# Kernel optimization log

Hardware: AMD Instinct MI355X
Metric: run time of the kernel (lower is better)

Reference implementation:

```python
import jax, jax.numpy as jnp
import numpy as np

B, H, S, D = 4, 16, 2048, 64

def setup_inputs() -> dict:
    key = jax.random.key(0)
    kq, kk, kv = jax.random.split(key, 3)
    q = jax.random.normal(kq, (B, H, S, D), dtype=jnp.float32)
    k = jax.random.normal(kk, (B, H, S, D), dtype=jnp.float32)
    v = jax.random.normal(kv, (B, H, S, D), dtype=jnp.float32)
    return {"q": q, "k": k, "v": v}

def reference(q, k, v):
    # dots: [b,h,i,j] = q . k (NO 1/sqrt(d) scaling, matching source)
    dots = jnp.einsum('bhid,bhjd->bhij', q, k)
    # causal=False (and the source's causal mask is a no-op bug anyway)
    attn = jax.nn.softmax(dots, axis=-1)
    # out: [b,h,i,d] = sum_j attn[b,h,i,j] * v[b,h,j,d]
    return jnp.einsum('bhjd,bhij->bhid', v, attn)
```

## Files before the change

kernel.cpp:

```cpp
#include <hip/hip_runtime.h>
#include <hip/hip_bf16.h>
#include <stdint.h>

#define B_ 4
#define H_ 16
#define S_ 2048
#define D_ 64
#define QBLK 128
#define KBLK 64
#define LDW 72
#define LOG2E 1.44269504088896340736f

typedef __attribute__((ext_vector_type(8))) short short8;
typedef __attribute__((ext_vector_type(4))) float f32x4;
typedef __attribute__((ext_vector_type(16))) float f32x16;
typedef _Float16 f16x8 __attribute__((ext_vector_type(8)));
typedef _Float16 f16x4 __attribute__((ext_vector_type(4)));
typedef __fp16 fp16x2 __attribute__((ext_vector_type(2)));

__device__ __forceinline__ unsigned short f2bf(float f) {
  union { float f; unsigned int u; } x; x.f = f;
  unsigned int u = x.u;
  unsigned int r = (u + 0x7FFFu + ((u >> 16) & 1u)) >> 16;
  return (unsigned short)r;
}
__device__ __forceinline__ float bf2f(unsigned short h) {
  union { unsigned int u; float f; } y; y.u = ((unsigned int)h) << 16;
  return y.f;
}

__device__ __forceinline__ unsigned pkrtz(float a, float b) {
  union { fp16x2 h; unsigned u; } c;
  c.h = __builtin_amdgcn_cvt_pkrtz(a, b);
  return c.u;
}
__device__ __forceinline__ fp16x2 u2h(unsigned u) {
  union { unsigned u; fp16x2 h; } c; c.u = u; return c.h;
}

__device__ __forceinline__ float fast_exp2(float x) {
#if __has_builtin(__builtin_amdgcn_exp2f)
  return __builtin_amdgcn_exp2f(x);
#else
  return exp2f(x);
#endif
}

__device__ __forceinline__ void swap32(unsigned &a, unsigned &b) {
#if __has_builtin(__builtin_amdgcn_permlane32_swap)
  typedef int i32x2 __attribute__((ext_vector_type(2)));
  i32x2 r = __builtin_amdgcn_permlane32_swap((int)a, (int)b, false, false);
  a = (unsigned)r[0]; b = (unsigned)r[1];
#else
  unsigned pa = (unsigned)__shfl_xor((int)a, 32);
  unsigned pb = (unsigned)__shfl_xor((int)b, 32);
  bool lo = (threadIdx.x & 32) == 0;
  unsigned r0 = lo ? a : pb;
  unsigned r1 = lo ? pa : b;
  a = r0; b = r1;
#endif
}

__device__ __forceinline__ float pairmax(float x) {
  unsigned a = __float_as_uint(x), b = a;
  swap32(a, b);
  return fmaxf(__uint_as_float(a), __uint_as_float(b));
}
__device__ __forceinline__ float pairsum(float x) {
  unsigned a = __float_as_uint(x), b = a;
  swap32(a, b);
  return __uint_as_float(a) + __uint_as_float(b);
}

#define GLOAD16(g, l) __builtin_amdgcn_global_load_lds( \
    (const __attribute__((address_space(1))) unsigned int*)(g), \
    (__attribute__((address_space(3))) unsigned int*)(l), 16, 0, 0)

__global__ void prep_k(const float* __restrict__ K, _Float16* __restrict__ Kp) {
  int e4 = (blockIdx.x * 256 + threadIdx.x) * 4;
  int bh  = e4 >> 17;
  int rem = e4 & 131071;
  int s   = rem >> 6;
  int d0  = rem & 63;
  const float4 kv = *(const float4*)(K + (size_t)e4);
  f16x4 h;
  h[0] = (_Float16)kv.x; h[1] = (_Float16)kv.y;
  h[2] = (_Float16)kv.z; h[3] = (_Float16)kv.w;
  size_t off = ((size_t)bh * S_ + s) * 128 + (unsigned)((d0 * 2) ^ ((s & 7) << 4));
  *(f16x4*)((char*)Kp + off) = h;
}

__global__ void prep_v(const float* __restrict__ V, _Float16* __restrict__ Vt) {
  __shared__ _Float16 tile[64][66];
  int bh = blockIdx.x >> 5;
  int st = blockIdx.x & 31;
  const float* Vb = V + ((size_t)bh * S_ + st * 64) * 64;
  int tid = threadIdx.x;
  #pragma unroll
  for (int i = 0; i < 4; ++i) {
    int idx = i * 1024 + tid * 4;
    int r = idx >> 6, c = idx & 63;
    float4 vv = *(const float4*)(Vb + (size_t)r * 64 + c);
    f16x4 o;
    o[0] = (_Float16)vv.x; o[1] = (_Float16)vv.y;
    o[2] = (_Float16)vv.z; o[3] = (_Float16)vv.w;
    *(f16x4*)&tile[r][c] = o;
  }
  __syncthreads();
  int chunk = tid & 15;
  int dbase = tid >> 4;
  size_t outb = (size_t)bh * (64 * S_ * 2) + (size_t)st * 128;
  #pragma unroll
  for (int i = 0; i < 4; ++i) {
    int d = dbase + i * 16;
    f16x4 o;
    o[0] = tile[chunk * 4 + 0][d];
    o[1] = tile[chunk * 4 + 1][d];
    o[2] = tile[chunk * 4 + 2][d];
    o[3] = tile[chunk * 4 + 3][d];
    size_t off = outb + (size_t)d * (S_ * 2) + (unsigned)((chunk * 8) ^ ((d & 7) << 4));
    *(f16x4*)((char*)Vt + off) = o;
  }
}

__global__ __launch_bounds__(256)
void attn_fwd4(const float* __restrict__ Q, const _Float16* __restrict__ Kg,
               const _Float16* __restrict__ Vg, float* __restrict__ O) {
  __shared__ char smem[32768];

  const int tid  = threadIdx.x;
  const int lane = tid & 63;
  const int wid  = tid >> 6;
  const int l31  = lane & 31;
  const int hi   = lane >> 5;

  const int qtile = blockIdx.x;
  const int bh    = blockIdx.y;

  const char* KB = (const char*)Kg + (size_t)bh * (S_ * 128);
  const char* VB = (const char*)Vg + (size_t)bh * (64 * S_ * 2);
  const float* Qb = Q + (size_t)bh * S_ * D_;
  float*       Ob = O + (size_t)bh * S_ * D_;

  const int qrow = qtile * QBLK + wid * 32 + l31;
  f16x8 qf[4];
  #pragma unroll
  for (int ds = 0; ds < 4; ++ds) {
    const float* qp = Qb + (size_t)qrow * D_ + ds * 16 + hi * 8;
    float4 a = *(const float4*)(qp);
    float4 b = *(const float4*)(qp + 4);
    qf[ds][0] = (_Float16)(a.x * LOG2E); qf[ds][1] = (_Float16)(a.y * LOG2E);
    qf[ds][2] = (_Float16)(a.z * LOG2E); qf[ds][3] = (_Float16)(a.w * LOG2E);
    qf[ds][4] = (_Float16)(b.x * LOG2E); qf[ds][5] = (_Float16)(b.y * LOG2E);
    qf[ds][6] = (_Float16)(b.z * LOG2E); qf[ds][7] = (_Float16)(b.w * LOG2E);
  }

  f32x16 oacc[2];
  #pragma unroll
  for (int dn = 0; dn < 2; ++dn)
    #pragma unroll
    for (int r = 0; r < 16; ++r) oacc[dn][r] = 0.f;
  float m_r = -INFINITY, l_r = 0.f;

  f32x16 zero16;
  #pragma unroll
  for (int r = 0; r < 16; ++r) zero16[r] = 0.f;

  #define STAGE(buf, kb)                                                        \
    {                                                                           \
      char* Kl_ = smem + (buf) * 16384;                                         \
      char* Vl_ = Kl_ + 8192;                                                   \
      _Pragma("unroll")                                                         \
      for (int c = 0; c < 4; ++c) {                                             \
        int id = c * 4 + wid;                                                   \
        if (id < 8) {                                                           \
          GLOAD16(KB + (size_t)(kb) * 128 + id * 1024 + lane * 16,              \
                  Kl_ + id * 1024);                                             \
        } else {                                                                \
          int i = id - 8;                                                       \
          GLOAD16(VB + (size_t)(i * 8 + (lane >> 3)) * (S_ * 2)                 \
                     + ((kb) >> 6) * 128 + (lane & 7) * 16,                     \
                  Vl_ + i * 1024);                                              \
        }                                                                       \
      }                                                                         \
    }

  STAGE(0, 0);
  __syncthreads();

  for (int it = 0; it < S_ / KBLK; ++it) {
    const int cur = it & 1;
    if (it < S_ / KBLK - 1) STAGE(cur ^ 1, (it + 1) * KBLK);

    const char* Kl = smem + cur * 16384;
    const char* Vl = Kl + 8192;

    f32x16 sacc_a, sacc_b;
    __builtin_amdgcn_s_setprio(1);
    {
      const int row = l31;
      const int sw = (row & 7) << 4;
      sacc_a = __builtin_amdgcn_mfma_f32_32x32x16_f16(
          *(const f16x8*)(Kl + row * 128 + ((0) ^ sw)), qf[0], zero16, 0, 0, 0);
      sacc_a = __builtin_amdgcn_mfma_f32_32x32x16_f16(
          *(const f16x8*)(Kl + row * 128 + ((32 + hi * 16) ^ sw) - hi * 16 + hi * 16), qf[1], sacc_a, 0, 0, 0);
      sacc_a = __builtin_amdgcn_mfma_f32_32x32x16_f16(
          *(const f16x8*)(Kl + row * 128 + ((64 + hi * 16) ^ sw) - hi * 16 + hi * 16), qf[2], sacc_a, 0, 0, 0);
      sacc_a = __builtin_amdgcn_mfma_f32_32x32x16_f16(
          *(const f16x8*)(Kl + row * 128 + ((96 + hi * 16) ^ sw) - hi * 16 + hi * 16), qf[3], sacc_a, 0, 0, 0);
    }
    __builtin_amdgcn_s_setprio(0);
    {
      const int row = l31;
      const int sw = (row & 7) << 4;
      sacc_a = __builtin_amdgcn_mfma_f32_32x32x16_f16(
          *(const f16x8*)(Kl + row * 128 + ((0 * 32 + hi * 16) ^ sw)), qf[0], zero16, 0, 0, 0);
      #pragma unroll
      for (int ds = 1; ds < 4; ++ds)
        sacc_a = __builtin_amdgcn_mfma_f32_32x32x16_f16(
            *(const f16x8*)(Kl + row * 128 + ((ds * 32 + hi * 16) ^ sw)), qf[ds], sacc_a, 0, 0, 0);
    }
    {
      const int row = 32 + l31;
      const int sw = (row & 7) << 4;
      sacc_b = __builtin_amdgcn_mfma_f32_32x32x16_f16(
          *(const f16x8*)(Kl + row * 128 + ((0 * 32 + hi * 16) ^ sw)), qf[0], zero16, 0, 0, 0);
      #pragma unroll
      for (int ds = 1; ds < 4; ++ds)
        sacc_b = __builtin_amdgcn_mfma_f32_32x32x16_f16(
            *(const f16x8*)(Kl + row * 128 + ((ds * 32 + hi * 16) ^ sw)), qf[ds], sacc_b, 0, 0, 0);
    }

    {
      float v0 = fmaxf(fmaxf(sacc_a[0], sacc_a[1]), sacc_a[2]);
      float v1 = fmaxf(fmaxf(sacc_a[3], sacc_a[4]), sacc_a[5]);
      float v2 = fmaxf(fmaxf(sacc_a[6], sacc_a[7]), sacc_a[8]);
      float v3 = fmaxf(fmaxf(sacc_a[9], sacc_a[10]), sacc_a[11]);
      float v4 = fmaxf(fmaxf(sacc_a[12], sacc_a[13]), sacc_a[14]);
      float w0 = fmaxf(fmaxf(v0, v1), v2);
      float w1 = fmaxf(fmaxf(v3, v4), sacc_a[15]);
      float mx = pairmax(fmaxf(w0, w1));
      if (!__all(mx <= m_r + 8.f)) {
        float nm = fmaxf(m_r, mx);
        float sc = fast_exp2(m_r - nm);
        m_r = nm; l_r *= sc;
        #pragma unroll
        for (int dn = 0; dn < 2; ++dn)
          #pragma unroll
          for (int r = 0; r < 16; ++r) oacc[dn][r] *= sc;
      }
      unsigned ww[8];
      #pragma unroll
      for (int r1 = 0; r1 < 4; ++r1) {
        float p0 = fast_exp2(sacc_a[4 * r1 + 0] - m_r);
        float p1 = fast_exp2(sacc_a[4 * r1 + 1] - m_r);
        float p2 = fast_exp2(sacc_a[4 * r1 + 2] - m_r);
        float p3 = fast_exp2(sacc_a[4 * r1 + 3] - m_r);
        ww[r1 * 2 + 0] = pkrtz(p0, p1);
        ww[r1 * 2 + 1] = pkrtz(p2, p3);
      }
      {
        const fp16x2 ones = {(__fp16)1.f, (__fp16)1.f};
        float rA = __builtin_amdgcn_fdot2(u2h(ww[0]), ones, 0.f, false);
        float rB = __builtin_amdgcn_fdot2(u2h(ww[1]), ones, 0.f, false);
        rA = __builtin_amdgcn_fdot2(u2h(ww[2]), ones, rA, false);
        rB = __builtin_amdgcn_fdot2(u2h(ww[3]), ones, rB, false);
        rA = __builtin_amdgcn_fdot2(u2h(ww[4]), ones, rA, false);
        rB = __builtin_amdgcn_fdot2(u2h(ww[5]), ones, rB, false);
        rA = __builtin_amdgcn_fdot2(u2h(ww[6]), ones, rA, false);
        rB = __builtin_amdgcn_fdot2(u2h(ww[7]), ones, rB, false);
        l_r += rA + rB;
      }
      f16x8 pb0, pb1;
      {
        unsigned u0 = ww[0], u1 = ww[1], u2 = ww[2], u3 = ww[3];
        swap32(u0, u2); swap32(u1, u3);
        union { unsigned u[4]; f16x8 v; } c;
        c.u[0] = u0; c.u[1] = u1; c.u[2] = u2; c.u[3] = u3;
        pb0 = c.v;
      }
      {
        unsigned u0 = ww[4], u1 = ww[5], u2 = ww[6], u3 = ww[7];
        swap32(u0, u2); swap32(u1, u3);
        union { unsigned u[4]; f16x8 v; } c;
        c.u[0] = u0; c.u[1] = u1; c.u[2] = u2; c.u[3] = u3;
        pb1 = c.v;
      }
      __builtin_amdgcn_s_setprio(1);
      #pragma unroll
      for (int dn = 0; dn < 2; ++dn) {
        const int d = dn * 32 + l31;
        const int sw = (d & 7) << 4;
        f16x8 vf0 = *(const f16x8*)(Vl + d * 128 + ((0 * 32 + hi * 16) ^ sw));
        f16x8 vf1 = *(const f16x8*)(Vl + d * 128 + ((1 * 32 + hi * 16) ^ sw));
        oacc[dn] = __builtin_amdgcn_mfma_f32_32x32x16_f16(vf0, pb0, oacc[dn], 0, 0, 0);
        oacc[dn] = __builtin_amdgcn_mfma_f32_32x32x16_f16(vf1, pb1, oacc[dn], 0, 0, 0);
      }
      __builtin_amdgcn_s_setprio(0);
    }

    {
      float v0 = fmaxf(fmaxf(sacc_b[0], sacc_b[1]), sacc_b[2]);
      float v1 = fmaxf(fmaxf(sacc_b[3], sacc_b[4]), sacc_b[5]);
      float v2 = fmaxf(fmaxf(sacc_b[6], sacc_b[7]), sacc_b[8]);
      float v3 = fmaxf(fmaxf(sacc_b[9], sacc_b[10]), sacc_b[11]);
      float v4 = fmaxf(fmaxf(sacc_b[12], sacc_b[13]), sacc_b[14]);
      float w0 = fmaxf(fmaxf(v0, v1), v2);
      float w1 = fmaxf(fmaxf(v3, v4), sacc_b[15]);
      float mx = pairmax(fmaxf(w0, w1));
      if (!__all(mx <= m_r + 8.f)) {
        float nm = fmaxf(m_r, mx);
        float sc = fast_exp2(m_r - nm);
        m_r = nm; l_r *= sc;
        #pragma unroll
        for (int dn = 0; dn < 2; ++dn)
          #pragma unroll
          for (int r = 0; r < 16; ++r) oacc[dn][r] *= sc;
      }
      unsigned ww[8];
      #pragma unroll
      for (int r1 = 0; r1 < 4; ++r1) {
        float p0 = fast_exp2(sacc_b[4 * r1 + 0] - m_r);
        float p1 = fast_exp2(sacc_b[4 * r1 + 1] - m_r);
        float p2 = fast_exp2(sacc_b[4 * r1 + 2] - m_r);
        float p3 = fast_exp2(sacc_b[4 * r1 + 3] - m_r);
        ww[r1 * 2 + 0] = pkrtz(p0, p1);
        ww[r1 * 2 + 1] = pkrtz(p2, p3);
      }
      {
        const fp16x2 ones = {(__fp16)1.f, (__fp16)1.f};
        float rA = __builtin_amdgcn_fdot2(u2h(ww[0]), ones, 0.f, false);
        float rB = __builtin_amdgcn_fdot2(u2h(ww[1]), ones, 0.f, false);
        rA = __builtin_amdgcn_fdot2(u2h(ww[2]), ones, rA, false);
        rB = __builtin_amdgcn_fdot2(u2h(ww[3]), ones, rB, false);
        rA = __builtin_amdgcn_fdot2(u2h(ww[4]), ones, rA, false);
        rB = __builtin_amdgcn_fdot2(u2h(ww[5]), ones, rB, false);
        rA = __builtin_amdgcn_fdot2(u2h(ww[6]), ones, rA, false);
        rB = __builtin_amdgcn_fdot2(u2h(ww[7]), ones, rB, false);
        l_r += rA + rB;
      }
      f16x8 pb2, pb3;
      {
        unsigned u0 = ww[0], u1 = ww[1], u2 = ww[2], u3 = ww[3];
        swap32(u0, u2); swap32(u1, u3);
        union { unsigned u[4]; f16x8 v; } c;
        c.u[0] = u0; c.u[1] = u1; c.u[2] = u2; c.u[3] = u3;
        pb2 = c.v;
      }
      {
        unsigned u0 = ww[4], u1 = ww[5], u2 = ww[6], u3 = ww[7];
        swap32(u0, u2); swap32(u1, u3);
        union { unsigned u[4]; f16x8 v; } c;
        c.u[0] = u0; c.u[1] = u1; c.u[2] = u2; c.u[3] = u3;
        pb3 = c.v;
      }
      __builtin_amdgcn_s_setprio(1);
      #pragma unroll
      for (int dn = 0; dn < 2; ++dn) {
        const int d = dn * 32 + l31;
        const int sw = (d & 7) << 4;
        f16x8 vf2 = *(const f16x8*)(Vl + d * 128 + ((2 * 32 + hi * 16) ^ sw));
        f16x8 vf3 = *(const f16x8*)(Vl + d * 128 + ((3 * 32 + hi * 16) ^ sw));
        oacc[dn] = __builtin_amdgcn_mfma_f32_32x32x16_f16(vf2, pb2, oacc[dn], 0, 0, 0);
        oacc[dn] = __builtin_amdgcn_mfma_f32_32x32x16_f16(vf3, pb3, oacc[dn], 0, 0, 0);
      }
      __builtin_amdgcn_s_setprio(0);
    }

    __syncthreads();
  }
  #undef STAGE

  const float inv = 1.0f / pairsum(l_r);
  float* Ep = (float*)(smem + wid * 8192);
  #pragma unroll
  for (int dn = 0; dn < 2; ++dn)
    #pragma unroll
    for (int r = 0; r < 16; ++r) {
      int d = dn * 32 + (r & 3) + 8 * (r >> 2) + 4 * hi;
      Ep[d * 32 + l31] = oacc[dn][r] * inv;
    }
  __syncthreads();
  const int q2 = lane >> 1, dh = lane & 1;
  float* orow = Ob + (size_t)(qtile * QBLK + wid * 32 + q2) * D_ + dh * 32;
  #pragma unroll
  for (int c = 0; c < 8; ++c) {
    float4 o4;
    o4.x = Ep[(dh * 32 + c * 4 + 0) * 32 + q2];
    o4.y = Ep[(dh * 32 + c * 4 + 1) * 32 + q2];
    o4.z = Ep[(dh * 32 + c * 4 + 2) * 32 + q2];
    o4.w = Ep[(dh * 32 + c * 4 + 3) * 32 + q2];
    *(float4*)(orow + c * 4) = o4;
  }
}

__global__ __launch_bounds__(256, 2)
void attn_fwd(const float* __restrict__ Q, const float* __restrict__ K,
              const float* __restrict__ V, float* __restrict__ O) {
  __shared__ alignas(16) unsigned short Kh_lds[KBLK * LDW];
  __shared__ alignas(16) unsigned short Kl_lds[KBLK * LDW];
  __shared__ alignas(16) unsigned short Vt_lds[D_ * LDW];
  __shared__ alignas(16) unsigned short P_lds[4][16 * LDW];

  const int tid  = threadIdx.x;
  const int lane = tid & 63;
  const int wid  = tid >> 6;
  const int l15  = lane & 15;
  const int dgrp = lane >> 4;

  const int qtile = blockIdx.x;
  const int bh    = blockIdx.y;

  const size_t base = (size_t)bh * S_ * D_;
  const float* Qb = Q + base;
  const float* Kb = K + base;
  const float* Vb = V + base;
  float*       Ob = O + base;

  const int qrow = qtile * 64 + wid * 16 + l15;
  short8 qfh[2], qfl[2];
  {
    const float* qp = Qb + (size_t)qrow * D_ + dgrp * 8;
    #pragma unroll
    for (int s = 0; s < 2; ++s)
      #pragma unroll
      for (int j = 0; j < 8; ++j) {
        float f = qp[s * 32 + j];
        unsigned short h = f2bf(f);
        qfh[s][j] = (short)h;
        qfl[s][j] = (short)f2bf(f - bf2f(h));
      }
  }

  f32x4 oacc[4];
  #pragma unroll
  for (int t = 0; t < 4; ++t) oacc[t] = f32x4{0.f, 0.f, 0.f, 0.f};
  float m_r[4], l_r[4];
  #pragma unroll
  for (int j = 0; j < 4; ++j) { m_r[j] = -INFINITY; l_r[j] = 0.f; }

  for (int kb = 0; kb < S_; kb += KBLK) {
    __syncthreads();
    #pragma unroll
    for (int c = 0; c < 4; ++c) {
      int e = (c * 256 + tid) * 4;
      int r = e >> 6, col = e & 63;
      const float4 kv = *(const float4*)(Kb + (size_t)(kb + r) * D_ + col);
      ushort4 kh, kl;
      kh.x = f2bf(kv.x); kl.x = f2bf(kv.x - bf2f(kh.x));
      kh.y = f2bf(kv.y); kl.y = f2bf(kv.y - bf2f(kh.y));
      kh.z = f2bf(kv.z); kl.z = f2bf(kv.z - bf2f(kh.z));
      kh.w = f2bf(kv.w); kl.w = f2bf(kv.w - bf2f(kh.w));
      *(ushort4*)&Kh_lds[r * LDW + col] = kh;
      *(ushort4*)&Kl_lds[r * LDW + col] = kl;
      const float4 vv = *(const float4*)(Vb + (size_t)(kb + r) * D_ + col);
      Vt_lds[(col + 0) * LDW + r] = f2bf(vv.x);
      Vt_lds[(col + 1) * LDW + r] = f2bf(vv.y);
      Vt_lds[(col + 2) * LDW + r] = f2bf(vv.z);
      Vt_lds[(col + 3) * LDW + r] = f2bf(vv.w);
    }
    __syncthreads();

    f32x4 sa[4];
    #pragma unroll
    for (int t = 0; t < 4; ++t) {
      sa[t] = f32x4{0.f, 0.f, 0.f, 0.f};
      #pragma unroll
      for (int s = 0; s < 2; ++s) {
        const int off = (t * 16 + l15) * LDW + s * 32 + dgrp * 8;
        short8 kfh = *(const short8*)&Kh_lds[off];
        short8 kfl = *(const short8*)&Kl_lds[off];
        sa[t] = __builtin_amdgcn_mfma_f32_16x16x32_bf16(qfh[s], kfh, sa[t], 0, 0, 0);
        sa[t] = __builtin_amdgcn_mfma_f32_16x16x32_bf16(qfh[s], kfl, sa[t], 0, 0, 0);
        sa[t] = __builtin_amdgcn_mfma_f32_16x16x32_bf16(qfl[s], kfh, sa[t], 0, 0, 0);
      }
    }

    float pmax[4];
    #pragma unroll
    for (int j = 0; j < 4; ++j) {
      float mx = fmaxf(fmaxf(sa[0][j], sa[1][j]), fmaxf(sa[2][j], sa[3][j]));
      #pragma unroll
      for (int m = 1; m < 16; m <<= 1) mx = fmaxf(mx, __shfl_xor(mx, m));
      pmax[j] = mx;
    }
    float scale[4];
    #pragma unroll
    for (int j = 0; j < 4; ++j) {
      float nm = fmaxf(m_r[j], pmax[j]);
      scale[j] = __expf(m_r[j] - nm);
      m_r[j] = nm;
    }
    float rs[4] = {0.f, 0.f, 0.f, 0.f};
    #pragma unroll
    for (int t = 0; t < 4; ++t)
      #pragma unroll
      for (int j = 0; j < 4; ++j) {
        float p = __expf(sa[t][j] - m_r[j]);
        rs[j] += p;
        P_lds[wid][(dgrp * 4 + j) * LDW + t * 16 + l15] = f2bf(p);
      }
    #pragma unroll
    for (int j = 0; j < 4; ++j) {
      #pragma unroll
      for (int m = 1; m < 16; m <<= 1) rs[j] += __shfl_xor(rs[j], m);
      l_r[j] = l_r[j] * scale[j] + rs[j];
      #pragma unroll
      for (int t = 0; t < 4; ++t) oacc[t][j] *= scale[j];
    }

    #pragma unroll
    for (int s = 0; s < 2; ++s) {
      short8 pf = *(const short8*)&P_lds[wid][l15 * LDW + s * 32 + dgrp * 8];
      #pragma unroll
      for (int t = 0; t < 4; ++t) {
        short8 vf = *(const short8*)&Vt_lds[(t * 16 + l15) * LDW + s * 32 + dgrp * 8];
        oacc[t] = __builtin_amdgcn_mfma_f32_16x16x32_bf16(pf, vf, oacc[t], 0, 0, 0);
      }
    }
  }

  #pragma unroll
  for (int j = 0; j < 4; ++j) {
    float inv = 1.0f / l_r[j];
    int row = qtile * 64 + wid * 16 + dgrp * 4 + j;
    float* op = Ob + (size_t)row * D_ + l15;
    #pragma unroll
    for (int t = 0; t < 4; ++t)
      op[t * 16] = oacc[t][j] * inv;
  }
}

extern "C" void kernel_launch(void* const* d_in, const int* in_sizes, int n_in,
                              void* d_out, int out_size, void* d_ws, size_t ws_size,
                              hipStream_t stream) {
  const float* q = (const float*)d_in[0];
  const float* k = (const float*)d_in[1];
  const float* v = (const float*)d_in[2];
  float* o = (float*)d_out;
  const size_t PLANE = (size_t)B_ * H_ * S_ * 128;
  if (ws_size >= 2 * PLANE) {
    _Float16* Kp = (_Float16*)d_ws;
    _Float16* Vt = (_Float16*)((char*)d_ws + PLANE);
    prep_k<<<8192, 256, 0, stream>>>(k, Kp);
    prep_v<<<2048, 256, 0, stream>>>(v, Vt);
    attn_fwd4<<<dim3(S_ / QBLK, B_ * H_), 256, 0, stream>>>(q, Kp, Vt, o);
  } else {
    attn_fwd<<<dim3(S_ / 64, B_ * H_), 256, 0, stream>>>(q, k, v, o);
  }
}
```

Before: 144.8 us.

## Software-pipeline QK^T one tile ahead with triple-buffered K/V LDS stages

Moves from double to triple buffering of K/V tiles in shared memory and computes the next tile's QK^T MFMAs before the current tile's softmax and PV work. The aim is to overlap matrix-core work with the softmax VALU work and to give global prefetches two iterations of lead time. It also drops a redundant duplicated QK computation that the old loop did. In exchange it uses 48KB of LDS per block, which may lower occupancy, and keeps two extra 16-float accumulators live, which raises register pressure.

After: 148.7 us. 2.7% more time.

```diff
diff --git a/kernel.cpp b/kernel.cpp
--- a/kernel.cpp
+++ b/kernel.cpp
@@ -8,6 +8,7 @@
 #define D_ 64
 #define QBLK 128
 #define KBLK 64
+#define NT (S_ / KBLK)
 #define LDW 72
 #define LOG2E 1.44269504088896340736f
 
@@ -124,9 +125,9 @@
 }
 
 __global__ __launch_bounds__(256)
-void attn_fwd4(const float* __restrict__ Q, const _Float16* __restrict__ Kg,
+void attn_fwd6(const float* __restrict__ Q, const _Float16* __restrict__ Kg,
                const _Float16* __restrict__ Vg, float* __restrict__ O) {
-  __shared__ char smem[32768];
+  __shared__ char smem[49152];
 
   const int tid  = threadIdx.x;
   const int lane = tid & 63;
@@ -166,9 +167,9 @@
   #pragma unroll
   for (int r = 0; r < 16; ++r) zero16[r] = 0.f;
 
-  #define STAGE(buf, kb)                                                        \
+  #define STAGE(base, kb)                                                       \
     {                                                                           \
-      char* Kl_ = smem + (buf) * 16384;                                         \
+      char* Kl_ = (base);                                                       \
       char* Vl_ = Kl_ + 8192;                                                   \
       _Pragma("unroll")                                                         \
       for (int c = 0; c < 4; ++c) {                                             \
@@ -185,51 +186,51 @@
       }                                                                         \
     }
 
-  STAGE(0, 0);
+  #define QKCOMP(dA, dB, Klp)                                                   \
+    {                                                                           \
+      const int row_a = l31;                                                    \
+      const int sw_a = (row_a & 7) << 4;                                        \
+      dA = __builtin_amdgcn_mfma_f32_32x32x16_f16(                              \
+          *(const f16x8*)((Klp) + row_a * 128 + ((hi * 16) ^ sw_a)),            \
+          qf[0], zero16, 0, 0, 0);                                              \
+      _Pragma("unroll")                                                         \
+      for (int ds = 1; ds < 4; ++ds)                                            \
+        dA = __builtin_amdgcn_mfma_f32_32x32x16_f16(                            \
+            *(const f16x8*)((Klp) + row_a * 128 + ((ds * 32 + hi * 16) ^ sw_a)),\
+            qf[ds], dA, 0, 0, 0);                                               \
+      const int row_b = 32 + l31;                                               \
+      const int sw_b = (row_b & 7) << 4;                                        \
+      dB = __builtin_amdgcn_mfma_f32_32x32x16_f16(                              \
+          *(const f16x8*)((Klp) + row_b * 128 + ((hi * 16) ^ sw_b)),            \
+          qf[0], zero16, 0, 0, 0);                                              \
+      _Pragma("unroll")                                                         \
+      for (int ds = 1; ds < 4; ++ds)                                            \
+        dB = __builtin_amdgcn_mfma_f32_32x32x16_f16(                            \
+            *(const f16x8*)((Klp) + row_b * 128 + ((ds * 32 + hi * 16) ^ sw_b)),\
+            qf[ds], dB, 0, 0, 0);                                               \
+    }
+
+  STAGE(smem, 0);
   __syncthreads();
-
-  for (int it = 0; it < S_ / KBLK; ++it) {
-    const int cur = it & 1;
-    if (it < S_ / KBLK - 1) STAGE(cur ^ 1, (it + 1) * KBLK);
-
-    const char* Kl = smem + cur * 16384;
-    const char* Vl = Kl + 8192;
-
-    f32x16 sacc_a, sacc_b;
-    __builtin_amdgcn_s_setprio(1);
-    {
-      const int row = l31;
-      const int sw = (row & 7) << 4;
-      sacc_a = __builtin_amdgcn_mfma_f32_32x32x16_f16(
-          *(const f16x8*)(Kl + row * 128 + ((0) ^ sw)), qf[0], zero16, 0, 0, 0);
-      sacc_a = __builtin_amdgcn_mfma_f32_32x32x16_f16(
-          *(const f16x8*)(Kl + row * 128 + ((32 + hi * 16) ^ sw) - hi * 16 + hi * 16), qf[1], sacc_a, 0, 0, 0);
-      sacc_a = __builtin_amdgcn_mfma_f32_32x32x16_f16(
-          *(const f16x8*)(Kl + row * 128 + ((64 + hi * 16) ^ sw) - hi * 16 + hi * 16), qf[2], sacc_a, 0, 0, 0);
-      sacc_a = __builtin_amdgcn_mfma_f32_32x32x16_f16(
-          *(const f16x8*)(Kl + row * 128 + ((96 + hi * 16) ^ sw) - hi * 16 + hi * 16), qf[3], sacc_a, 0, 0, 0);
-    }
-    __builtin_amdgcn_s_setprio(0);
-    {
-      const int row = l31;
-      const int sw = (row & 7) << 4;
-      sacc_a = __builtin_amdgcn_mfma_f32_32x32x16_f16(
-          *(const f16x8*)(Kl + row * 128 + ((0 * 32 + hi * 16) ^ sw)), qf[0], zero16, 0, 0, 0);
-      #pragma unroll
-      for (int ds = 1; ds < 4; ++ds)
-        sacc_a = __builtin_amdgcn_mfma_f32_32x32x16_f16(
-            *(const f16x8*)(Kl + row * 128 + ((ds * 32 + hi * 16) ^ sw)), qf[ds], sacc_a, 0, 0, 0);
-    }
-    {
-      const int row = 32 + l31;
-      const int sw = (row & 7) << 4;
-      sacc_b = __builtin_amdgcn_mfma_f32_32x32x16_f16(
-          *(const f16x8*)(Kl + row * 128 + ((0 * 32 + hi * 16) ^ sw)), qf[0], zero16, 0, 0, 0);
-      #pragma unroll
-      for (int ds = 1; ds < 4; ++ds)
-        sacc_b = __builtin_amdgcn_mfma_f32_32x32x16_f16(
-            *(const f16x8*)(Kl + row * 128 + ((ds * 32 + hi * 16) ^ sw)), qf[ds], sacc_b, 0, 0, 0);
-    }
+  STAGE(smem + 16384, KBLK);
+  f32x16 sacc_a, sacc_b;
+  __builtin_amdgcn_s_setprio(1);
+  QKCOMP(sacc_a, sacc_b, smem);
+  __builtin_amdgcn_s_setprio(0);
+  __syncthreads();
+
+  int cur = 0, nxt = 1, pre = 2;
+  for (int it = 0; it < NT; ++it) {
+    if (it + 2 < NT) STAGE(smem + pre * 16384, (it + 2) * KBLK);
+
+    f32x16 snA, snB;
+    if (it + 1 < NT) {
+      __builtin_amdgcn_s_setprio(1);
+      QKCOMP(snA, snB, smem + nxt * 16384);
+      __builtin_amdgcn_s_setprio(0);
+    }
+
+    const char* Vl = smem + cur * 16384 + 8192;
 
     {
       float v0 = fmaxf(fmaxf(sacc_a[0], sacc_a[1]), sacc_a[2]);
@@ -367,9 +368,12 @@
       __builtin_amdgcn_s_setprio(0);
     }
 
+    if (it + 1 < NT) { sacc_a = snA; sacc_b = snB; }
     __syncthreads();
+    int t = cur; cur = nxt; nxt = pre; pre = t;
   }
   #undef STAGE
+  #undef QKCOMP
 
   const float inv = 1.0f / pairsum(l_r);
   float* Ep = (float*)(smem + wid * 8192);
@@ -544,7 +548,7 @@
     _Float16* Vt = (_Float16*)((char*)d_ws + PLANE);
     prep_k<<<8192, 256, 0, stream>>>(k, Kp);
     prep_v<<<2048, 256, 0, stream>>>(v, Vt);
-    attn_fwd4<<<dim3(S_ / QBLK, B_ * H_), 256, 0, stream>>>(q, Kp, Vt, o);
+    attn_fwd6<<<dim3(S_ / QBLK, B_ * H_), 256, 0, stream>>>(q, Kp, Vt, o);
   } else {
     attn_fwd<<<dim3(S_ / 64, B_ * H_), 256, 0, stream>>>(q, k, v, o);
   }
```
